# Performance work log

Measured on AMD Instinct MI355X. Metric: run time of the kernel, lower is better.

## Reference

```python
import jax, jax.numpy as jnp
import numpy as np

D_MODEL, N_HEADS, LATENT, ROPE = 4096, 128, 512, 64
HEAD_DIM = D_MODEL // N_HEADS  # 32
B, S = 2, 1024


def setup_inputs() -> dict:
    key = jax.random.key(0)
    ks = jax.random.split(key, 9)
    def w(k, i, o):
        return jax.random.normal(k, (i, o), dtype=jnp.float32) * (1.0 / np.sqrt(i))
    return {
        "x": jax.random.normal(ks[0], (B, S, D_MODEL), dtype=jnp.float32),
        "Wq_down": w(ks[1], D_MODEL, LATENT),
        "Wq_up": w(ks[2], LATENT, N_HEADS * HEAD_DIM),
        "Wq_rope": w(ks[3], D_MODEL, N_HEADS * ROPE),
        "Wkv_down": w(ks[4], D_MODEL, LATENT),
        "Wk_up": w(ks[5], LATENT, N_HEADS * HEAD_DIM),
        "Wv_up": w(ks[6], LATENT, N_HEADS * HEAD_DIM),
        "Wk_rope": w(ks[7], D_MODEL, ROPE),
        "Wo": w(ks[8], N_HEADS * HEAD_DIM, D_MODEL),
    }


def reference(x, Wq_down, Wq_up, Wq_rope, Wkv_down, Wk_up, Wv_up, Wk_rope, Wo):
    b, s, _ = x.shape
    # latent down-projections
    c_q = x @ Wq_down                                   # [B,S,latent]
    c_kv = x @ Wkv_down                                 # [B,S,latent]
    # up-projections, reshaped to per-head
    q_c = (c_q @ Wq_up).reshape(b, s, N_HEADS, HEAD_DIM)    # [B,S,H,Dh]
    q_r = (x @ Wq_rope).reshape(b, s, N_HEADS, ROPE)        # [B,S,H,Dr]
    k_c = (c_kv @ Wk_up).reshape(b, s, N_HEADS, HEAD_DIM)   # [B,S,H,Dh]
    v_c = (c_kv @ Wv_up).reshape(b, s, N_HEADS, HEAD_DIM)   # [B,S,H,Dh]
    k_r = x @ Wk_rope                                       # [B,S,Dr] shared over heads
    scale = jnp.asarray((HEAD_DIM + ROPE) ** 0.5, x.dtype)
    # scores = q.k with q=[q_c|q_r], k=[k_c|k_r(broadcast)] -> split the dot product
    scores = (jnp.einsum("bqhd,bkhd->bhqk", q_c, k_c)
              + jnp.einsum("bqhd,bkd->bhqk", q_r, k_r)) / scale  # [B,H,S,S]
    attn = jax.nn.softmax(scores, axis=-1)
    out = jnp.einsum("bhqk,bkhd->bqhd", attn, v_c)          # [B,S,H,Dh]
    out = out.reshape(b, s, N_HEADS * HEAD_DIM)
    return out @ Wo                                         # [B,S,d_model]
```

## Files before the change

kernel.cpp:

```cpp
#include <hip/hip_runtime.h>
#include <hip/hip_bf16.h>
#include <math.h>

#define D_MODEL 4096
#define N_HEADS 128
#define LATENT  512
#define ROPE_D  64
#define HEAD_D  32
#define BATCH   2
#define SEQ     1024
#define NTOK    (BATCH*SEQ)

typedef unsigned short u16;
typedef __attribute__((ext_vector_type(8))) short bf16x8;
typedef __attribute__((ext_vector_type(4))) float f32x4;

__device__ __forceinline__ u16 f2bf(float f) {
    union { float f; unsigned u; } v; v.f = f;
    unsigned r = (v.u + 0x7fffu + ((v.u >> 16) & 1u)) >> 16;
    return (u16)r;
}

__device__ __forceinline__ void gl_lds16(const u16* g, u16* l) {
    __builtin_amdgcn_global_load_lds(
        (const __attribute__((address_space(1))) unsigned int*)g,
        (__attribute__((address_space(3))) unsigned int*)l, 16, 0, 0);
}

__global__ __launch_bounds__(256)
void cast_x_kernel(const float* __restrict__ in, u16* __restrict__ out)
{
    size_t i = ((size_t)blockIdx.x * 256 + threadIdx.x) * 8;
    float4 a = *(const float4*)(in + i);
    float4 b = *(const float4*)(in + i + 4);
    u16 o[8] = {f2bf(a.x), f2bf(a.y), f2bf(a.z), f2bf(a.w),
                f2bf(b.x), f2bf(b.y), f2bf(b.z), f2bf(b.w)};
    *(bf16x8*)(out + i) = *(bf16x8*)o;
}

__global__ __launch_bounds__(256)
void castT_kernel(const float* __restrict__ W, u16* __restrict__ Wt,
                  int K, int N)
{
    __shared__ float tile[32][33];
    const int tid = threadIdx.x;
    const int j0 = blockIdx.x * 32;
    const int i0 = blockIdx.y * 32;
    #pragma unroll
    for (int it = 0; it < 4; ++it) {
        int e = tid + it * 256;
        int r = e >> 5, c = e & 31;
        tile[r][c] = (j0 + c < N) ? W[(size_t)(i0 + r) * N + j0 + c] : 0.f;
    }
    __syncthreads();
    #pragma unroll
    for (int it = 0; it < 4; ++it) {
        int e = tid + it * 256;
        int n = e >> 5, k = e & 31;
        Wt[(size_t)(j0 + n) * K + i0 + k] = f2bf(tile[k][n]);
    }
}

template<int OUTF32>
__global__ __launch_bounds__(256)
void gemm_bf16(const u16* __restrict__ A, const u16* __restrict__ Bt,
               void* __restrict__ Cout, int M, int N, int K,
               int lda, int ldb, int ldc)
{
    __shared__ __align__(16) u16 As[128 * 64];
    __shared__ __align__(16) u16 Bs[128 * 64];

    const int tid  = threadIdx.x;
    const int lane = tid & 63;
    const int wave = tid >> 6;
    const int wr = wave >> 1, wc = wave & 1;
    const int nwg  = gridDim.x * gridDim.y;
    const int orig = blockIdx.y * gridDim.x + blockIdx.x;
    const int swz  = (orig & 7) * (nwg >> 3) + (orig >> 3);
    const int bm = (swz / gridDim.x) * 128, bn = (swz % gridDim.x) * 128;
    const int l15 = lane & 15, lg = lane >> 4;

    f32x4 acc[4][4];
    #pragma unroll
    for (int i = 0; i < 4; ++i)
        #pragma unroll
        for (int j = 0; j < 4; ++j) acc[i][j] = (f32x4){0.f, 0.f, 0.f, 0.f};

    for (int kt = 0; kt < K; kt += 64) {
        __syncthreads();
        #pragma unroll
        for (int i = 0; i < 4; ++i) {
            int f = i * 256 + tid;
            int row = f >> 3, c = f & 7;
            int sc = c ^ (row & 7);
            gl_lds16(A + (size_t)(bm + row) * lda + kt + sc * 8, As + f * 8);
        }
        #pragma unroll
        for (int i = 0; i < 4; ++i) {
            int f = i * 256 + tid;
            int row = f >> 3, c = f & 7;
            int sc = c ^ (row & 7);
            gl_lds16(Bt + (size_t)(bn + row) * ldb + kt + sc * 8, Bs + f * 8);
        }
        __syncthreads();

        #pragma unroll
        for (int t = 0; t < 2; ++t) {
            bf16x8 af[4], bf[4];
            #pragma unroll
            for (int fm = 0; fm < 4; ++fm) {
                int row = wr * 64 + fm * 16 + l15;
                int c = (t * 4 + lg) ^ (row & 7);
                af[fm] = *(const bf16x8*)(As + row * 64 + c * 8);
            }
            #pragma unroll
            for (int fn = 0; fn < 4; ++fn) {
                int row = wc * 64 + fn * 16 + l15;
                int c = (t * 4 + lg) ^ (row & 7);
                bf[fn] = *(const bf16x8*)(Bs + row * 64 + c * 8);
            }
            #pragma unroll
            for (int fm = 0; fm < 4; ++fm)
                #pragma unroll
                for (int fn = 0; fn < 4; ++fn)
                    acc[fm][fn] = __builtin_amdgcn_mfma_f32_16x16x32_bf16(
                        af[fm], bf[fn], acc[fm][fn], 0, 0, 0);
        }
    }

    #pragma unroll
    for (int fm = 0; fm < 4; ++fm)
        #pragma unroll
        for (int fn = 0; fn < 4; ++fn)
            #pragma unroll
            for (int ri = 0; ri < 4; ++ri) {
                int row = bm + wr * 64 + fm * 16 + 4 * lg + ri;
                int col = bn + wc * 64 + fn * 16 + l15;
                if (col < N) {
                    float v = acc[fm][fn][ri];
                    if (OUTF32) ((float*)Cout)[(size_t)row * ldc + col] = v;
                    else        ((u16*)Cout)[(size_t)row * ldc + col] = f2bf(v);
                }
            }
}

__global__ __launch_bounds__(256)
void vtrans_kernel(const u16* __restrict__ vc, u16* __restrict__ vt)
{
    __shared__ __align__(16) u16 tile[64][72];
    const int tid = threadIdx.x;
    const int c0 = blockIdx.x * 64;
    const int s0 = blockIdx.y * 64;
    const int b  = blockIdx.z;
    #pragma unroll
    for (int it = 0; it < 2; ++it) {
        int e = it * 256 + tid;
        int r = e >> 3, c8 = e & 7;
        *(bf16x8*)&tile[r][c8 * 8] =
            *(const bf16x8*)(vc + (size_t)(b * SEQ + s0 + r) * 8192 + c0 + c8 * 8);
    }
    __syncthreads();
    #pragma unroll
    for (int it = 0; it < 2; ++it) {
        int e = it * 256 + tid;
        int d = e >> 3, c8 = e & 7;
        u16 o[8];
        #pragma unroll
        for (int j = 0; j < 8; ++j) o[j] = tile[c8 * 8 + j][d];
        *(bf16x8*)(vt + (size_t)(b * D_MODEL + c0 + d) * SEQ + s0 + c8 * 8) = *(bf16x8*)o;
    }
}

__global__ __launch_bounds__(256)
void attn_kernel(const u16* __restrict__ q_c, const u16* __restrict__ q_r,
                 const u16* __restrict__ k_c, const u16* __restrict__ k_r,
                 const u16* __restrict__ vt,  u16* __restrict__ attn_out)
{
    __shared__ __align__(16) u16 s_kc[2][64 * 32];
    __shared__ __align__(16) u16 s_kr[2][64 * 64];
    __shared__ __align__(16) u16 s_vt[2][32 * 64];
    __shared__ __align__(16) u16 s_p[4][16 * 64];

    const int tid  = threadIdx.x;
    const int lane = tid & 63;
    const int w    = tid >> 6;
    const int l15  = lane & 15, lg = lane >> 4;
    const int q0 = blockIdx.x * 64;
    const int h  = blockIdx.y;
    const int b  = blockIdx.z;
    const size_t bS = (size_t)b * SEQ;
    const int hc = h * HEAD_D;
    const float c2 = 0.1020620726159658f * 1.44269504088896f;

    const int qrow = q0 + w * 16 + l15;
    const bf16x8 qf0 = *(const bf16x8*)(q_c + (bS + qrow) * 4096 + hc + lg * 8);
    const bf16x8 qf1 = *(const bf16x8*)(q_r + (bS + qrow) * 9344 + h * ROPE_D + lg * 8);
    const bf16x8 qf2 = *(const bf16x8*)(q_r + (bS + qrow) * 9344 + h * ROPE_D + 32 + lg * 8);

    float m2 = -1e30f, lsum = 0.f;
    f32x4 oacc[2];
    oacc[0] = (f32x4){0.f, 0.f, 0.f, 0.f};
    oacc[1] = (f32x4){0.f, 0.f, 0.f, 0.f};

    auto stage = [&](int buf, int k0) {
        { int f = tid, r = f >> 2, c = f & 3;
          gl_lds16(k_c + (bS + k0 + r) * 8192 + hc + ((c ^ (r & 3)) << 3),
                   &s_kc[buf][f * 8]); }
        #pragma unroll
        for (int it = 0; it < 2; ++it) {
          int f = it * 256 + tid, r = f >> 3, c = f & 7;
          gl_lds16(k_r + (bS + k0 + r) * 9344 + ((c ^ (r & 7)) << 3),
                   &s_kr[buf][f * 8]); }
        { int f = tid, d = f >> 3, c = f & 7;
          gl_lds16(vt + ((size_t)b * D_MODEL + hc + d) * SEQ + k0 + ((c ^ (d & 7)) << 3),
                   &s_vt[buf][f * 8]); }
    };

    stage(0, 0);
    __syncthreads();

    int cur = 0;
    for (int t = 0; t < SEQ / 64; ++t) {
        if (t + 1 < SEQ / 64) stage(cur ^ 1, (t + 1) * 64);

        f32x4 sc[4];
        #pragma unroll
        for (int fc = 0; fc < 4; ++fc) sc[fc] = (f32x4){0.f, 0.f, 0.f, 0.f};
        __builtin_amdgcn_s_setprio(1);
        #pragma unroll
        for (int fc = 0; fc < 4; ++fc) {
            int row = fc * 16 + l15;
            bf16x8 kb = *(const bf16x8*)&s_kc[cur][row * 32 + ((lg ^ (row & 3)) << 3)];
            sc[fc] = __builtin_amdgcn_mfma_f32_16x16x32_bf16(kb, qf0, sc[fc], 0, 0, 0);
        }
        #pragma unroll
        for (int tt = 0; tt < 2; ++tt) {
            bf16x8 qf = tt ? qf2 : qf1;
            #pragma unroll
            for (int fc = 0; fc < 4; ++fc) {
                int row = fc * 16 + l15;
                bf16x8 kb = *(const bf16x8*)&s_kr[cur][row * 64 + (((tt * 4 + lg) ^ (row & 7)) << 3)];
                sc[fc] = __builtin_amdgcn_mfma_f32_16x16x32_bf16(kb, qf, sc[fc], 0, 0, 0);
            }
        }
        __builtin_amdgcn_s_setprio(0);

        float tmx = sc[0][0];
        #pragma unroll
        for (int fc = 0; fc < 4; ++fc)
            #pragma unroll
            for (int ri = 0; ri < 4; ++ri)
                tmx = fmaxf(tmx, sc[fc][ri]);
        tmx = fmaxf(tmx, __shfl_xor(tmx, 16));
        tmx = fmaxf(tmx, __shfl_xor(tmx, 32));
        float tl2 = tmx * c2;
        if (!__all(tl2 <= m2 + 8.f)) {
            float mn = fmaxf(m2, tl2);
            float corr = exp2f(m2 - mn);
            m2 = mn;
            lsum *= corr;
            #pragma unroll
            for (int ri = 0; ri < 4; ++ri) {
                float cr = __shfl(corr, 4 * lg + ri);
                oacc[0][ri] *= cr; oacc[1][ri] *= cr;
            }
        }
        float rs = 0.f;
        unsigned pk0[4], pk1[4];
        #pragma unroll
        for (int fc = 0; fc < 4; ++fc) {
            float p0 = exp2f(fmaf(sc[fc][0], c2, -m2));
            float p1 = exp2f(fmaf(sc[fc][1], c2, -m2));
            float p2 = exp2f(fmaf(sc[fc][2], c2, -m2));
            float p3 = exp2f(fmaf(sc[fc][3], c2, -m2));
            rs += (p0 + p1) + (p2 + p3);
            asm("v_cvt_pk_bf16_f32 %0, %1, %2" : "=v"(pk0[fc]) : "v"(p0), "v"(p1));
            asm("v_cvt_pk_bf16_f32 %0, %1, %2" : "=v"(pk1[fc]) : "v"(p2), "v"(p3));
        }
        rs += __shfl_xor(rs, 16);
        rs += __shfl_xor(rs, 32);
        lsum += rs;
        #pragma unroll
        for (int fc = 0; fc < 4; ++fc) {
            int ch = (2 * fc + (lg >> 1)) ^ (l15 & 7);
            *(uint2*)&s_p[w][l15 * 64 + ch * 8 + 4 * (lg & 1)] =
                make_uint2(pk0[fc], pk1[fc]);
        }

        __builtin_amdgcn_s_setprio(1);
        #pragma unroll
        for (int t2 = 0; t2 < 2; ++t2) {
            bf16x8 pa = *(const bf16x8*)&s_p[w][l15 * 64 + (((t2 * 4 + lg) ^ (l15 & 7)) << 3)];
            #pragma unroll
            for (int fd = 0; fd < 2; ++fd) {
                int row = fd * 16 + l15;
                bf16x8 vb = *(const bf16x8*)&s_vt[cur][row * 64 + (((t2 * 4 + lg) ^ (row & 7)) << 3)];
                oacc[fd] = __builtin_amdgcn_mfma_f32_16x16x32_bf16(pa, vb, oacc[fd], 0, 0, 0);
            }
        }
        __builtin_amdgcn_s_setprio(0);

        __syncthreads();
        cur ^= 1;
    }

    #pragma unroll
    for (int ri = 0; ri < 4; ++ri) {
        float ls = __shfl(lsum, 4 * lg + ri);
        float inv = 1.f / ls;
        int row = q0 + w * 16 + 4 * lg + ri;
        attn_out[(bS + row) * 4096 + hc + l15]      = f2bf(oacc[0][ri] * inv);
        attn_out[(bS + row) * 4096 + hc + 16 + l15] = f2bf(oacc[1][ri] * inv);
    }
}

extern "C" void kernel_launch(void* const* d_in, const int* in_sizes, int n_in,
                              void* d_out, int out_size, void* d_ws, size_t ws_size,
                              hipStream_t stream)
{
    (void)in_sizes; (void)n_in; (void)out_size; (void)ws_size;

    const float* x        = (const float*)d_in[0];
    const float* Wq_down  = (const float*)d_in[1];
    const float* Wq_up    = (const float*)d_in[2];
    const float* Wq_rope  = (const float*)d_in[3];
    const float* Wkv_down = (const float*)d_in[4];
    const float* Wk_up    = (const float*)d_in[5];
    const float* Wv_up    = (const float*)d_in[6];
    const float* Wk_rope  = (const float*)d_in[7];
    const float* Wo       = (const float*)d_in[8];

    u16* ws   = (u16*)d_ws;
    u16* xb   = ws;
    u16* BigT = xb + (size_t)8388608;
    u16* UpT  = BigT + (size_t)38273024;
    u16* WuqT = UpT + (size_t)4194304;
    u16* C_big= WuqT + (size_t)2097152;
    u16* C2   = C_big + (size_t)19136512;
    u16* WoT  = BigT;
    u16* vt   = BigT + (size_t)16777216;
    u16* q_c  = BigT + (size_t)25165824;
    u16* attn_out = xb;

    dim3 blk(256);

    hipMemsetAsync(BigT + (size_t)9280 * 4096, 0, (size_t)64 * 4096 * 2, stream);
    hipLaunchKernelGGL(cast_x_kernel, dim3(4096), blk, 0, stream, x, xb);
    hipLaunchKernelGGL(castT_kernel, dim3(256, 128), blk, 0, stream, Wq_rope, BigT, 4096, 8192);
    hipLaunchKernelGGL(castT_kernel, dim3(16, 128), blk, 0, stream, Wq_down, BigT + (size_t)8192 * 4096, 4096, 512);
    hipLaunchKernelGGL(castT_kernel, dim3(16, 128), blk, 0, stream, Wkv_down, BigT + (size_t)8704 * 4096, 4096, 512);
    hipLaunchKernelGGL(castT_kernel, dim3(2, 128), blk, 0, stream, Wk_rope, BigT + (size_t)9216 * 4096, 4096, 64);
    hipLaunchKernelGGL(castT_kernel, dim3(128, 16), blk, 0, stream, Wk_up, UpT, 512, 4096);
    hipLaunchKernelGGL(castT_kernel, dim3(128, 16), blk, 0, stream, Wv_up, UpT + (size_t)4096 * 512, 512, 4096);
    hipLaunchKernelGGL(castT_kernel, dim3(128, 16), blk, 0, stream, Wq_up, WuqT, 512, 4096);

    gemm_bf16<0><<<dim3(73, 16), blk, 0, stream>>>(xb, BigT, C_big, NTOK, 9344, 4096, 4096, 4096, 9344);
    hipLaunchKernelGGL(castT_kernel, dim3(128, 128), blk, 0, stream, Wo, WoT, 4096, 4096);
    gemm_bf16<0><<<dim3(64, 16), blk, 0, stream>>>(C_big + 8704, UpT, C2, NTOK, 8192, 512, 9344, 512, 8192);
    gemm_bf16<0><<<dim3(32, 16), blk, 0, stream>>>(C_big + 8192, WuqT, q_c, NTOK, 4096, 512, 9344, 512, 4096);
    hipLaunchKernelGGL(vtrans_kernel, dim3(64, 16, 2), blk, 0, stream, C2 + 4096, vt);
    hipLaunchKernelGGL(attn_kernel, dim3(16, 128, 2), blk, 0, stream,
                       q_c, C_big, C2, C_big + 9216, vt, attn_out);
    gemm_bf16<1><<<dim3(32, 16), blk, 0, stream>>>(attn_out, WoT, d_out, NTOK, 4096, 4096, 4096, 4096, 4096);
}
```

Before: 594.8 us.

## Merge prep casts into one launch, fuse up-proj GEMMs with Wo cast, fine-grained attn sync

All weight casts, the x cast and the zero-padding memset now run in a single prep launch, and the castT tile uses vectorized float4 loads and uint2 stores. The two up-projection GEMMs and the Wo transpose-cast share one launch, with bm/bn derived in column-major swizzle order. The attention loop replaces __syncthreads with explicit vmcnt waits plus barriers, so the next tile's prefetch can stay in flight while the current one computes. Together these cut launch overhead and improve overlap, but the GEMM column bounds check is removed and the vmcnt counts are hand-tuned.

```diff
diff --git a/kernel.cpp b/kernel.cpp
--- a/kernel.cpp
+++ b/kernel.cpp
@@ -27,57 +27,39 @@
         (__attribute__((address_space(3))) unsigned int*)l, 16, 0, 0);
 }
 
-__global__ __launch_bounds__(256)
-void cast_x_kernel(const float* __restrict__ in, u16* __restrict__ out)
-{
-    size_t i = ((size_t)blockIdx.x * 256 + threadIdx.x) * 8;
-    float4 a = *(const float4*)(in + i);
-    float4 b = *(const float4*)(in + i + 4);
-    u16 o[8] = {f2bf(a.x), f2bf(a.y), f2bf(a.z), f2bf(a.w),
-                f2bf(b.x), f2bf(b.y), f2bf(b.z), f2bf(b.w)};
-    *(bf16x8*)(out + i) = *(bf16x8*)o;
-}
-
-__global__ __launch_bounds__(256)
-void castT_kernel(const float* __restrict__ W, u16* __restrict__ Wt,
-                  int K, int N)
-{
-    __shared__ float tile[32][33];
+__device__ __forceinline__ void castT_tile(const float* __restrict__ W,
+                                           u16* __restrict__ Wt,
+                                           int K, int N, int jx, int jy,
+                                           float (*tile)[33])
+{
     const int tid = threadIdx.x;
-    const int j0 = blockIdx.x * 32;
-    const int i0 = blockIdx.y * 32;
-    #pragma unroll
-    for (int it = 0; it < 4; ++it) {
-        int e = tid + it * 256;
-        int r = e >> 5, c = e & 31;
-        tile[r][c] = (j0 + c < N) ? W[(size_t)(i0 + r) * N + j0 + c] : 0.f;
+    const int j0 = jx * 32, i0 = jy * 32;
+    {
+        int r = tid >> 3, c4 = (tid & 7) << 2;
+        float4 v = *(const float4*)(W + (size_t)(i0 + r) * N + j0 + c4);
+        tile[r][c4 + 0] = v.x; tile[r][c4 + 1] = v.y;
+        tile[r][c4 + 2] = v.z; tile[r][c4 + 3] = v.w;
     }
     __syncthreads();
-    #pragma unroll
-    for (int it = 0; it < 4; ++it) {
-        int e = tid + it * 256;
-        int n = e >> 5, k = e & 31;
-        Wt[(size_t)(j0 + n) * K + i0 + k] = f2bf(tile[k][n]);
-    }
-}
-
-template<int OUTF32>
-__global__ __launch_bounds__(256)
-void gemm_bf16(const u16* __restrict__ A, const u16* __restrict__ Bt,
-               void* __restrict__ Cout, int M, int N, int K,
-               int lda, int ldb, int ldc)
-{
-    __shared__ __align__(16) u16 As[128 * 64];
-    __shared__ __align__(16) u16 Bs[128 * 64];
-
+    {
+        int n = tid >> 3, k4 = (tid & 7) << 2;
+        u16 o[4] = { f2bf(tile[k4 + 0][n]), f2bf(tile[k4 + 1][n]),
+                     f2bf(tile[k4 + 2][n]), f2bf(tile[k4 + 3][n]) };
+        *(uint2*)(Wt + (size_t)(j0 + n) * K + i0 + k4) = *(uint2*)o;
+    }
+}
+
+__device__ __forceinline__ void gemm_core(const u16* __restrict__ A,
+                                          const u16* __restrict__ Bt,
+                                          void* __restrict__ Cout,
+                                          int N, int K, int lda, int ldb, int ldc,
+                                          int bm, int bn, u16* As, u16* Bs,
+                                          int OUTF32)
+{
     const int tid  = threadIdx.x;
     const int lane = tid & 63;
     const int wave = tid >> 6;
     const int wr = wave >> 1, wc = wave & 1;
-    const int nwg  = gridDim.x * gridDim.y;
-    const int orig = blockIdx.y * gridDim.x + blockIdx.x;
-    const int swz  = (orig & 7) * (nwg >> 3) + (orig >> 3);
-    const int bm = (swz / gridDim.x) * 128, bn = (swz % gridDim.x) * 128;
     const int l15 = lane & 15, lg = lane >> 4;
 
     f32x4 acc[4][4];
@@ -136,12 +118,98 @@
             for (int ri = 0; ri < 4; ++ri) {
                 int row = bm + wr * 64 + fm * 16 + 4 * lg + ri;
                 int col = bn + wc * 64 + fn * 16 + l15;
-                if (col < N) {
-                    float v = acc[fm][fn][ri];
-                    if (OUTF32) ((float*)Cout)[(size_t)row * ldc + col] = v;
-                    else        ((u16*)Cout)[(size_t)row * ldc + col] = f2bf(v);
-                }
-            }
+                float v = acc[fm][fn][ri];
+                if (OUTF32) ((float*)Cout)[(size_t)row * ldc + col] = v;
+                else        ((u16*)Cout)[(size_t)row * ldc + col] = f2bf(v);
+            }
+}
+
+template<int OUTF32>
+__global__ __launch_bounds__(256)
+void gemm_bf16(const u16* __restrict__ A, const u16* __restrict__ Bt,
+               void* __restrict__ Cout, int N, int K,
+               int lda, int ldb, int ldc)
+{
+    __shared__ __align__(16) u16 As[128 * 64];
+    __shared__ __align__(16) u16 Bs[128 * 64];
+    const int nwg  = gridDim.x * gridDim.y;
+    const int orig = blockIdx.y * gridDim.x + blockIdx.x;
+    const int swz  = (orig & 7) * (nwg >> 3) + (orig >> 3);
+    const int bm = (swz % gridDim.y) * 128;
+    const int bn = (swz / gridDim.y) * 128;
+    gemm_core(A, Bt, Cout, N, K, lda, ldb, ldc, bm, bn, As, Bs, OUTF32);
+}
+
+__global__ __launch_bounds__(256)
+void prep_kernel(const float* __restrict__ x, u16* __restrict__ xb,
+                 const float* __restrict__ Wq_rope, const float* __restrict__ Wq_down,
+                 const float* __restrict__ Wkv_down, const float* __restrict__ Wk_rope,
+                 const float* __restrict__ Wk_up, const float* __restrict__ Wv_up,
+                 const float* __restrict__ Wq_up,
+                 u16* __restrict__ BigT, u16* __restrict__ UpT, u16* __restrict__ WuqT)
+{
+    __shared__ float tile[32][33];
+    const int tid = threadIdx.x;
+    int id = blockIdx.x;
+    if (id < 4096) {
+        size_t i = ((size_t)id * 256 + tid) * 8;
+        float4 a = *(const float4*)(x + i);
+        float4 b = *(const float4*)(x + i + 4);
+        u16 o[8] = {f2bf(a.x), f2bf(a.y), f2bf(a.z), f2bf(a.w),
+                    f2bf(b.x), f2bf(b.y), f2bf(b.z), f2bf(b.w)};
+        *(bf16x8*)(xb + i) = *(bf16x8*)o;
+        return;
+    }
+    id -= 4096;
+    if (id < 32768) { castT_tile(Wq_rope, BigT, 4096, 8192, id & 255, id >> 8, tile); return; }
+    id -= 32768;
+    if (id < 2048) { castT_tile(Wq_down, BigT + (size_t)8192 * 4096, 4096, 512, id & 15, id >> 4, tile); return; }
+    id -= 2048;
+    if (id < 2048) { castT_tile(Wkv_down, BigT + (size_t)8704 * 4096, 4096, 512, id & 15, id >> 4, tile); return; }
+    id -= 2048;
+    if (id < 256) { castT_tile(Wk_rope, BigT + (size_t)9216 * 4096, 4096, 64, id & 1, id >> 1, tile); return; }
+    id -= 256;
+    if (id < 2048) { castT_tile(Wk_up, UpT, 512, 4096, id & 127, id >> 7, tile); return; }
+    id -= 2048;
+    if (id < 2048) { castT_tile(Wv_up, UpT + (size_t)4096 * 512, 512, 4096, id & 127, id >> 7, tile); return; }
+    id -= 2048;
+    if (id < 2048) { castT_tile(Wq_up, WuqT, 512, 4096, id & 127, id >> 7, tile); return; }
+    id -= 2048;
+    {
+        u16* dst = BigT + ((size_t)9280 + id) * 4096;
+        bf16x8 z = (bf16x8){0, 0, 0, 0, 0, 0, 0, 0};
+        *(bf16x8*)(dst + tid * 8) = z;
+        *(bf16x8*)(dst + 2048 + tid * 8) = z;
+    }
+}
+
+__global__ __launch_bounds__(256)
+void fused2_kernel(const u16* __restrict__ Cbig, const u16* __restrict__ UpT,
+                   u16* __restrict__ C2, const u16* __restrict__ WuqT,
+                   u16* __restrict__ q_c, const float* __restrict__ Wo,
+                   u16* __restrict__ WoT)
+{
+    __shared__ __align__(16) u16 As[128 * 64];
+    __shared__ __align__(16) u16 Bs[128 * 64];
+    int id = blockIdx.x;
+    if (id < 1024) {
+        const int swz = (id & 7) * 128 + (id >> 3);
+        const int bm = (swz & 15) * 128, bn = (swz >> 4) * 128;
+        gemm_core(Cbig + 8704, UpT, C2, 8192, 512, 9344, 512, 8192, bm, bn, As, Bs, 0);
+        return;
+    }
+    id -= 1024;
+    if (id < 512) {
+        const int swz = (id & 7) * 64 + (id >> 3);
+        const int bm = (swz & 15) * 128, bn = (swz >> 4) * 128;
+        gemm_core(Cbig + 8192, WuqT, q_c, 4096, 512, 9344, 512, 4096, bm, bn, As, Bs, 0);
+        return;
+    }
+    id -= 512;
+    {
+        float (*tile)[33] = reinterpret_cast<float(*)[33]>(As);
+        castT_tile(Wo, WoT, 4096, 4096, id & 127, id >> 7, tile);
+    }
 }
 
 __global__ __launch_bounds__(256)
@@ -217,11 +285,22 @@
     };
 
     stage(0, 0);
-    __syncthreads();
+    asm volatile("s_waitcnt vmcnt(0)" ::: "memory");
+    __builtin_amdgcn_sched_barrier(0);
+    __builtin_amdgcn_s_barrier();
+    __builtin_amdgcn_sched_barrier(0);
 
     int cur = 0;
     for (int t = 0; t < SEQ / 64; ++t) {
-        if (t + 1 < SEQ / 64) stage(cur ^ 1, (t + 1) * 64);
+        if (t + 1 < SEQ / 64) {
+            stage(cur ^ 1, (t + 1) * 64);
+            asm volatile("s_waitcnt vmcnt(4)" ::: "memory");
+        } else {
+            asm volatile("s_waitcnt vmcnt(0)" ::: "memory");
+        }
+        __builtin_amdgcn_sched_barrier(0);
+        __builtin_amdgcn_s_barrier();
+        __builtin_amdgcn_sched_barrier(0);
 
         f32x4 sc[4];
         #pragma unroll
@@ -300,7 +379,10 @@
         }
         __builtin_amdgcn_s_setprio(0);
 
-        __syncthreads();
+        asm volatile("s_waitcnt lgkmcnt(0)" ::: "memory");
+        __builtin_amdgcn_sched_barrier(0);
+        __builtin_amdgcn_s_barrier();
+        __builtin_amdgcn_sched_barrier(0);
         cur ^= 1;
     }
 
@@ -333,7 +415,7 @@
     u16* ws   = (u16*)d_ws;
     u16* xb   = ws;
     u16* BigT = xb + (size_t)8388608;
-    u16* UpT  = BigT + (size_t)38273024;
+    u16* UpT  = BigT + (size_t)38797312;
     u16* WuqT = UpT + (size_t)4194304;
     u16* C_big= WuqT + (size_t)2097152;
     u16* C2   = C_big + (size_t)19136512;
@@ -344,22 +426,16 @@
 
     dim3 blk(256);
 
-    hipMemsetAsync(BigT + (size_t)9280 * 4096, 0, (size_t)64 * 4096 * 2, stream);
-    hipLaunchKernelGGL(cast_x_kernel, dim3(4096), blk, 0, stream, x, xb);
-    hipLaunchKernelGGL(castT_kernel, dim3(256, 128), blk, 0, stream, Wq_rope, BigT, 4096, 8192);
-    hipLaunchKernelGGL(castT_kernel, dim3(16, 128), blk, 0, stream, Wq_down, BigT + (size_t)8192 * 4096, 4096, 512);
-    hipLaunchKernelGGL(castT_kernel, dim3(16, 128), blk, 0, stream, Wkv_down, BigT + (size_t)8704 * 4096, 4096, 512);
-    hipLaunchKernelGGL(castT_kernel, dim3(2, 128), blk, 0, stream, Wk_rope, BigT + (size_t)9216 * 4096, 4096, 64);
-    hipLaunchKernelGGL(castT_kernel, dim3(128, 16), blk, 0, stream, Wk_up, UpT, 512, 4096);
-    hipLaunchKernelGGL(castT_kernel, dim3(128, 16), blk, 0, stream, Wv_up, UpT + (size_t)4096 * 512, 512, 4096);
-    hipLaunchKernelGGL(castT_kernel, dim3(128, 16), blk, 0, stream, Wq_up, WuqT, 512, 4096);
-
-    gemm_bf16<0><<<dim3(73, 16), blk, 0, stream>>>(xb, BigT, C_big, NTOK, 9344, 4096, 4096, 4096, 9344);
-    hipLaunchKernelGGL(castT_kernel, dim3(128, 128), blk, 0, stream, Wo, WoT, 4096, 4096);
-    gemm_bf16<0><<<dim3(64, 16), blk, 0, stream>>>(C_big + 8704, UpT, C2, NTOK, 8192, 512, 9344, 512, 8192);
-    gemm_bf16<0><<<dim3(32, 16), blk, 0, stream>>>(C_big + 8192, WuqT, q_c, NTOK, 4096, 512, 9344, 512, 4096);
+    hipLaunchKernelGGL(prep_kernel, dim3(47424), blk, 0, stream,
+                       x, xb, Wq_rope, Wq_down, Wkv_down, Wk_rope,
+                       Wk_up, Wv_up, Wq_up, BigT, UpT, WuqT);
+    gemm_bf16<0><<<dim3(73, 16), blk, 0, stream>>>(
+        xb, BigT, C_big, 9344, 4096, 4096, 4096, 9344);
+    hipLaunchKernelGGL(fused2_kernel, dim3(1024 + 512 + 16384), blk, 0, stream,
+                       C_big, UpT, C2, WuqT, q_c, Wo, WoT);
     hipLaunchKernelGGL(vtrans_kernel, dim3(64, 16, 2), blk, 0, stream, C2 + 4096, vt);
     hipLaunchKernelGGL(attn_kernel, dim3(16, 128, 2), blk, 0, stream,
                        q_c, C_big, C2, C_big + 9216, vt, attn_out);
-    gemm_bf16<1><<<dim3(32, 16), blk, 0, stream>>>(attn_out, WoT, d_out, NTOK, 4096, 4096, 4096, 4096, 4096);
-}
+    gemm_bf16<1><<<dim3(32, 16), blk, 0, stream>>>(
+        attn_out, WoT, d_out, 4096, 4096, 4096, 4096, 4096);
+}
```

Measured after the change: 512.7 us. -13.8%, faster.
